# Kernel optimization log

Hardware: AMD Instinct MI355X
Metric: run time of the kernel (lower is better)

The kernel has to match this reference:

```python
import jax, jax.numpy as jnp
import numpy as np

# ---- static config (from init_kwargs) ----
SAMPLE_RATE = 2048.0
MAX_SHIFT = int(0.025 * SAMPLE_RATE)          # 51 samples
NUM_BINS = 16
FFTLENGTH = 1.0                               # chisq_kernel_length (s)
DF = 1.0 / FFTLENGTH
NUM_FREQS = int(FFTLENGTH * SAMPLE_RATE // 2 + 1)   # 1025 == rfft bins of 2048 samples
HIGHPASS = 32.0
CHISQ_PENALTY = 1.0
_freqs = np.arange(NUM_FREQS) / FFTLENGTH
MASK = _freqs >= HIGHPASS                     # static numpy bool mask

BATCH, CHANNELS, DIM = 256, 2, 2048


def setup_inputs() -> dict:
    key = jax.random.key(0)
    k1, k2 = jax.random.split(key)
    x_hat = jax.random.normal(k1, (BATCH, CHANNELS, DIM), dtype=jnp.float32)
    x = jax.random.normal(k2, (BATCH, CHANNELS, DIM), dtype=jnp.float32)
    return {"x_hat": x_hat, "x": x}


def _center(x):
    xmin = x.min(-1, keepdims=True)
    xmax = x.max(-1, keepdims=True)
    return 2 * (x - xmin) / (xmax - xmin) - 1


def _shifted_pearson(x, y, max_shift):
    # x, y: [B, C, T]; returns corr: [W, B, C] with W = 2*max_shift + 1
    b, c, t = x.shape
    num_windows = 2 * max_shift + 1
    xp = jnp.pad(x, ((0, 0), (0, 0), (max_shift, max_shift)))
    # window w, position i -> xp[..., i + w]  (same layout as torch unfold)
    idx = jnp.arange(num_windows)[:, None] + jnp.arange(t)[None, :]   # [W, T]
    xw = xp[:, :, idx]                                                # [B, C, W, T]
    xw = jnp.transpose(xw, (2, 0, 1, 3))                              # [W, B, C, T]
    xw = xw - xw.mean(-1, keepdims=True)
    yc = y - y.mean(-1, keepdims=True)
    corr = (xw * yc).sum(-1)
    norm = (xw ** 2).sum(-1) * (yc ** 2).sum(-1)
    return corr / jnp.sqrt(norm)


def _snr_integral(a, b):
    # |4 * a * conj(b) * df| cumulatively summed over frequency
    integrand = a * jnp.conj(b)
    return jnp.abs(4 * integrand * DF).cumsum(-1)


def _chisq(htilde, stilde):
    htilde = htilde[:, :, MASK]
    stilde = stilde[:, :, MASK]
    # partition frequencies by the template's own optimal-SNR integral
    si = _snr_integral(htilde, htilde)                    # [B, C, F]
    total = si[:, :, -1:]
    bins = (jnp.arange(NUM_BINS + 1, dtype=si.dtype) / NUM_BINS) * total  # [B, C, NB+1]
    search = jax.vmap(jax.vmap(lambda a, v: jnp.searchsorted(a, v, side="right")))
    edges = search(si, bins)
    edges = jnp.clip(edges, 0, si.shape[-1] - 1)
    qtilde = htilde / jnp.sqrt(total).astype(htilde.dtype)
    # SNR per bin of the normalized template against the strain
    si2 = _snr_integral(qtilde, stilde)                   # [B, C, F]
    total2 = si2[:, :, -1:]
    right = jnp.take_along_axis(si2, edges[:, :, 1:], axis=-1)
    left = jnp.take_along_axis(si2, edges[:, :, :-1], axis=-1)
    snr_per_bin = right - left                            # [B, C, NB]
    summand = (snr_per_bin - total2 / NUM_BINS) ** 2
    chisq = NUM_BINS * summand.sum(-1) / (NUM_BINS - 1)
    return total2[:, :, 0], chisq


def reference(x_hat, x):
    x_hat = _center(x_hat)
    corr = _shifted_pearson(x_hat, x, MAX_SHIFT)          # [W, B, C]
    corr = corr.max(0)                                    # [B, C]
    loss = (1 - corr) / (1 + corr)
    htilde = jnp.fft.rfft(x_hat, axis=-1) / SAMPLE_RATE   # [B, C, 1025] complex
    stilde = jnp.fft.rfft(x, axis=-1) / SAMPLE_RATE
    _, chisq = _chisq(htilde, stilde)
    chisq = chisq * CHISQ_PENALTY
    loss = loss * (1 + chisq ** 3) ** (1.0 / 6.0)
    return loss
```

## Files before the change

kernel.cpp:

```cpp
#include <hip/hip_runtime.h>
#include <math.h>

#define ROWS 512
#define DIM 2048
#define MS 51
#define NWIN 103
#define KMIN 32
#define NMASK 993

__global__ __launch_bounds__(512) void fused_mfl_kernel(
    const float* __restrict__ xhat, const float* __restrict__ x,
    float* __restrict__ out)
{
    const int r = blockIdx.x;
    const int t = threadIdx.x;
    const int lane = t & 63;
    const int wave = t >> 6;

    __shared__ float smem[13056];
    float2* A2  = (float2*)smem;
    float2* B2  = (float2*)(smem + 4096);
    float2* TW  = (float2*)(smem + 8192);
    float2* Qlo = (float2*)smem;
    float2* Qhi = (float2*)smem + 1024;
    float* siA  = smem + 4096;
    float* siBr = smem + 5120;
    float* red6 = smem + 9216;
    float* ah   = smem + 12288;
    float* xhd  = smem + 12339;
    float* at_  = smem + 12390;
    float* xt_  = smem + 12441;
    float* Ah   = smem + 12492;
    float* Aqh  = smem + 12544;
    float* Xh   = smem + 12596;
    float* At   = smem + 12648;
    float* Aqt  = smem + 12700;
    float* Xt   = smem + 12752;
    float* corrv= smem + 12804;
    float* accv = smem + 12907;

    __shared__ float sc[8];
    __shared__ int   edges[17];
    __shared__ float summ[16];
    __shared__ float wsA[4], wsB[4];

    const float* xhp = xhat + (size_t)r * DIM;
    const float* xrp = x    + (size_t)r * DIM;
    float av[4] = {xhp[t], xhp[t+512], xhp[t+1024], xhp[t+1536]};
    float bv[4] = {xrp[t], xrp[t+512], xrp[t+1024], xrp[t+1536]};

    float swv, cwv;
    sincosf((float)t * (-3.14159265358979323846f / 1024.0f), &swv, &cwv);
    TW[t] = make_float2(cwv, swv);

    {
        float mn4 = fminf(fminf(av[0],av[1]), fminf(av[2],av[3]));
        float mx4 = fmaxf(fmaxf(av[0],av[1]), fmaxf(av[2],av[3]));
        float sa = (av[0]+av[1])+(av[2]+av[3]);
        float qa = (av[0]*av[0]+av[1]*av[1])+(av[2]*av[2]+av[3]*av[3]);
        float sx = (bv[0]+bv[1])+(bv[2]+bv[3]);
        float qx = (bv[0]*bv[0]+bv[1]*bv[1])+(bv[2]*bv[2]+bv[3]*bv[3]);
        red6[t] = mn4; red6[512+t] = mx4; red6[1024+t] = sa;
        red6[1536+t] = qa; red6[2048+t] = sx; red6[2560+t] = qx;
    }
    if (t < MS)   { ah[t] = av[0];      xhd[t] = bv[0]; }
    if (t >= 461) { at_[t-461] = av[3]; xt_[t-461] = bv[3]; }
    {
        float t0r=av[0]+av[2], t0i=bv[0]+bv[2];
        float t1r=av[0]-av[2], t1i=bv[0]-bv[2];
        float t2r=av[1]+av[3], t2i=bv[1]+bv[3];
        float d3r=av[1]-av[3], d3i=bv[1]-bv[3];
        float t3r=d3i, t3i=-d3r;
        float w1r=cwv, w1i=swv;
        float w2r=w1r*w1r-w1i*w1i, w2i=2.f*w1r*w1i;
        float w3r=w2r*w1r-w2i*w1i, w3i=w2r*w1i+w2i*w1r;
        float y0r=t0r+t2r, y0i=t0i+t2i;
        float a1r=t1r+t3r, a1i=t1i+t3i;
        float y1r=a1r*w1r-a1i*w1i, y1i=a1r*w1i+a1i*w1r;
        float a2r=t0r-t2r, a2i=t0i-t2i;
        float y2r=a2r*w2r-a2i*w2i, y2i=a2r*w2i+a2i*w2r;
        float a3r=t1r-t3r, a3i=t1i-t3i;
        float y3r=a3r*w3r-a3i*w3i, y3i=a3r*w3i+a3i*w3r;
        B2[4*t]   = make_float2(y0r,y0i);
        B2[4*t+1] = make_float2(y1r,y1i);
        B2[4*t+2] = make_float2(y2r,y2i);
        B2[4*t+3] = make_float2(y3r,y3i);
    }
    __syncthreads();

    auto fft2048 = [&](const float2* Sp, float2* Dp, const int s) {
        const int q = t;
        const int u = q & ~(s - 1);
        float2 x0 = Sp[q], x1 = Sp[q+512], x2 = Sp[q+1024], x3 = Sp[q+1536];
        float t0r=x0.x+x2.x, t0i=x0.y+x2.y;
        float t1r=x0.x-x2.x, t1i=x0.y-x2.y;
        float t2r=x1.x+x3.x, t2i=x1.y+x3.y;
        float d3r=x1.x-x3.x, d3i=x1.y-x3.y;
        float t3r=d3i, t3i=-d3r;
        float2 w1 = TW[u];
        float w2r=w1.x*w1.x-w1.y*w1.y, w2i=2.f*w1.x*w1.y;
        float w3r=w2r*w1.x-w2i*w1.y,  w3i=w2r*w1.y+w2i*w1.x;
        float y0r=t0r+t2r, y0i=t0i+t2i;
        float a1r=t1r+t3r, a1i=t1i+t3i;
        float y1r=a1r*w1.x-a1i*w1.y, y1i=a1r*w1.y+a1i*w1.x;
        float a2r=t0r-t2r, a2i=t0i-t2i;
        float y2r=a2r*w2r-a2i*w2i, y2i=a2r*w2i+a2i*w2r;
        float a3r=t1r-t3r, a3i=t1i-t3i;
        float y3r=a3r*w3r-a3i*w3i, y3i=a3r*w3i+a3i*w3r;
        int base = q + 3*u;
        Dp[base]     = make_float2(y0r,y0i);
        Dp[base+s]   = make_float2(y1r,y1i);
        Dp[base+2*s] = make_float2(y2r,y2i);
        Dp[base+3*s] = make_float2(y3r,y3i);
    };
    auto fft1024 = [&](const float2* Sp, float2* Dp, const int s) {
        const int q = t;
        const int u = q & ~(s - 1);
        float2 x0 = Sp[q], x1 = Sp[q+256], x2 = Sp[q+512], x3 = Sp[q+768];
        float t0r=x0.x+x2.x, t0i=x0.y+x2.y;
        float t1r=x0.x-x2.x, t1i=x0.y-x2.y;
        float t2r=x1.x+x3.x, t2i=x1.y+x3.y;
        float d3r=x1.x-x3.x, d3i=x1.y-x3.y;
        float t3r=d3i, t3i=-d3r;
        float2 w1 = TW[2*u];
        float w2r=w1.x*w1.x-w1.y*w1.y, w2i=2.f*w1.x*w1.y;
        float w3r=w2r*w1.x-w2i*w1.y,  w3i=w2r*w1.y+w2i*w1.x;
        float y0r=t0r+t2r, y0i=t0i+t2i;
        float a1r=t1r+t3r, a1i=t1i+t3i;
        float y1r=a1r*w1.x-a1i*w1.y, y1i=a1r*w1.y+a1i*w1.x;
        float a2r=t0r-t2r, a2i=t0i-t2i;
        float y2r=a2r*w2r-a2i*w2i, y2i=a2r*w2i+a2i*w2r;
        float a3r=t1r-t3r, a3i=t1i-t3i;
        float y3r=a3r*w3r-a3i*w3i, y3i=a3r*w3i+a3i*w3r;
        int base = q + 3*u;
        Dp[base]     = make_float2(y0r,y0i);
        Dp[base+s]   = make_float2(y1r,y1i);
        Dp[base+2*s] = make_float2(y2r,y2i);
        Dp[base+3*s] = make_float2(y3r,y3i);
    };

    fft2048(B2, A2, 4);
    if (wave == 0) {
        float4 u, v;
        u=((const float4*)(red6     ))[2*lane]; v=((const float4*)(red6     ))[2*lane+1];
        float pmn=fminf(fminf(fminf(u.x,u.y),fminf(u.z,u.w)),fminf(fminf(v.x,v.y),fminf(v.z,v.w)));
        u=((const float4*)(red6+ 512))[2*lane]; v=((const float4*)(red6+ 512))[2*lane+1];
        float pmx=fmaxf(fmaxf(fmaxf(u.x,u.y),fmaxf(u.z,u.w)),fmaxf(fmaxf(v.x,v.y),fmaxf(v.z,v.w)));
        u=((const float4*)(red6+1024))[2*lane]; v=((const float4*)(red6+1024))[2*lane+1];
        float psa=((u.x+u.y)+(u.z+u.w))+((v.x+v.y)+(v.z+v.w));
        u=((const float4*)(red6+1536))[2*lane]; v=((const float4*)(red6+1536))[2*lane+1];
        float pqa=((u.x+u.y)+(u.z+u.w))+((v.x+v.y)+(v.z+v.w));
        u=((const float4*)(red6+2048))[2*lane]; v=((const float4*)(red6+2048))[2*lane+1];
        float psx=((u.x+u.y)+(u.z+u.w))+((v.x+v.y)+(v.z+v.w));
        u=((const float4*)(red6+2560))[2*lane]; v=((const float4*)(red6+2560))[2*lane+1];
        float pqx=((u.x+u.y)+(u.z+u.w))+((v.x+v.y)+(v.z+v.w));
#pragma unroll
        for (int d = 32; d; d >>= 1) {
            pmn=fminf(pmn,__shfl_down(pmn,d)); pmx=fmaxf(pmx,__shfl_down(pmx,d));
            psa+=__shfl_down(psa,d); pqa+=__shfl_down(pqa,d);
            psx+=__shfl_down(psx,d); pqx+=__shfl_down(pqx,d);
        }
        if (lane == 0) {
            float scl = 2.0f/(pmx - pmn);
            float Cc  = scl*pmn + 1.0f;
            float mean = psx * (1.0f/DIM);
            sc[0]=scl; sc[1]=Cc; sc[2]=mean; sc[3]=psa; sc[4]=pqa;
            sc[5]=pqx - (float)DIM*mean*mean;
        }
    } else if (wave == 2) {
        float va=0.f, vq=0.f, vx=0.f;
        if (lane >= 1 && lane <= MS) { float aa=ah[lane-1]; va=aa; vq=aa*aa; vx=xhd[lane-1]; }
#pragma unroll
        for (int d = 1; d < 64; d <<= 1) {
            float ya=__shfl_up(va,d), yq=__shfl_up(vq,d), yx=__shfl_up(vx,d);
            if (lane >= d) { va+=ya; vq+=yq; vx+=yx; }
        }
        if (lane <= MS) { Ah[lane]=va; Aqh[lane]=vq; Xh[lane]=vx; }
    } else if (wave == 3) {
        float va=0.f, vq=0.f, vx=0.f;
        if (lane >= 1 && lane <= MS) { float aa=at_[MS-lane]; va=aa; vq=aa*aa; vx=xt_[MS-lane]; }
#pragma unroll
        for (int d = 1; d < 64; d <<= 1) {
            float ya=__shfl_up(va,d), yq=__shfl_up(vq,d), yx=__shfl_up(vx,d);
            if (lane >= d) { va+=ya; vq+=yq; vx+=yx; }
        }
        if (lane <= MS) { At[lane]=va; Aqt[lane]=vq; Xt[lane]=vx; }
    }
    __syncthreads();
    fft2048(A2, B2, 16);  __syncthreads();
    fft2048(B2, A2, 64);  __syncthreads();
    fft2048(A2, B2, 256); __syncthreads();

    const float scl = sc[0], Cc = sc[1], mean = sc[2];
    const float Sa = sc[3], Qa = sc[4], Szz = sc[5];
    const float MSC = 0.5f * (1.0f / 2048.0f);

    float se0=0,se1=0,se2=0,se3=0, sg0=0,sg1=0,sg2=0,sg3=0;
    float incE=0, incG=0, totE=0, totG=0;

    if (t < 256) {
        const int q = t;
        float2 wA = TW[q], wB = TW[q + 256];
        auto mkQ = [&](int k, float2 w, int ni) -> float2 {
            float2 Pa, Pb;
            if (k == 0) {
                float2 U = B2[0], V = B2[1024];
                float drx = U.x - V.x, dry = U.y - V.y;
                Pa = make_float2(0.f, 0.f);
                Pb = make_float2(4.f * drx * dry, 0.f);
            } else {
                float2 U = B2[k], V = B2[k + 1024];
                float2 R = B2[1024 - k], T = B2[2048 - k];
                float zfr = U.x + V.x, zfi = U.y + V.y;
                float zgr = R.x - T.x, zgi = R.y - T.y;
                float hre = zfr + zgr, him = zfi - zgi;
                float sre = zfi + zgi, sim = zgr - zfr;
                Pa = make_float2(hre*sre + him*sim, -(him*sre - hre*sim));
                float zfr2 = R.x + T.x, zfi2 = R.y + T.y;
                float zgr2 = U.x - V.x, zgi2 = U.y - V.y;
                float hre2 = zfr2 + zgr2, him2 = zfi2 - zgi2;
                float sre2 = zfi2 + zgi2, sim2 = zgr2 - zfr2;
                Pb = make_float2(hre2*sre2 + him2*sim2, him2*sre2 - hre2*sim2);
            }
            float D1r = Pa.x + Pb.x, D1i = Pa.y + Pb.y;
            float D2r = Pa.x - Pb.x, D2i = Pa.y - Pb.y;
            float Er = D2r*w.x - D2i*w.y;
            float Ei = D2r*w.y + D2i*w.x;
            if (ni) return make_float2(D1r - Er, D1i - Ei);
            return make_float2(D1r + Ei, D1i - Er);
        };
        float2 x0 = mkQ(q,     wA, 0);
        float2 x1 = mkQ(q+256, wB, 0);
        float2 x2 = mkQ(q+512, wA, 1);
        float2 x3 = mkQ(q+768, wB, 1);
        float t0r=x0.x+x2.x, t0i=x0.y+x2.y;
        float t1r=x0.x-x2.x, t1i=x0.y-x2.y;
        float t2r=x1.x+x3.x, t2i=x1.y+x3.y;
        float d3r=x1.x-x3.x, d3i=x1.y-x3.y;
        float t3r=d3i, t3i=-d3r;
        float2 w1 = TW[2*q];
        float w2r=w1.x*w1.x-w1.y*w1.y, w2i=2.f*w1.x*w1.y;
        float w3r=w2r*w1.x-w2i*w1.y,  w3i=w2r*w1.y+w2i*w1.x;
        float y0r=t0r+t2r, y0i=t0i+t2i;
        float a1r=t1r+t3r, a1i=t1i+t3i;
        float y1r=a1r*w1.x-a1i*w1.y, y1i=a1r*w1.y+a1i*w1.x;
        float a2r=t0r-t2r, a2i=t0i-t2i;
        float y2r=a2r*w2r-a2i*w2i, y2i=a2r*w2i+a2i*w2r;
        float a3r=t1r-t3r, a3i=t1i-t3i;
        float y3r=a3r*w3r-a3i*w3i, y3i=a3r*w3i+a3i*w3r;
        Qlo[4*q]   = make_float2(y0r,y0i);
        Qlo[4*q+1] = make_float2(y1r,y1i);
        Qlo[4*q+2] = make_float2(y2r,y2i);
        Qlo[4*q+3] = make_float2(y3r,y3i);
    } else {
        int tt = t - 256;
        float ee[4], gg[4];
#pragma unroll
        for (int j = 0; j < 4; ++j) {
            int m = 4*tt + j;
            ee[j] = 0.f; gg[j] = 0.f;
            if (m < NMASK) {
                int f = m + KMIN;
                float zfr, zfi;
                if (f < 1024) { float2 U=B2[f], V=B2[f+1024]; zfr=U.x+V.x; zfi=U.y+V.y; }
                else          { float2 U=B2[0], V=B2[1024];   zfr=U.x-V.x; zfi=U.y-V.y; }
                int gi = 2048 - f;
                float2 p2 = B2[gi-1024], q3 = B2[gi];
                float zgr = p2.x - q3.x, zgi = p2.y - q3.y;
                float hre = zfr + zgr, him = zfi - zgi;
                float sre = zfi + zgi, sim = zgr - zfr;
                float hm = scl * sqrtf(hre*hre + him*him) * MSC;
                float sm = sqrtf(sre*sre + sim*sim) * MSC;
                ee[j] = 4.f*hm*hm; gg[j] = 4.f*hm*sm;
            }
        }
        se0=ee[0]; se1=se0+ee[1]; se2=se1+ee[2]; se3=se2+ee[3];
        sg0=gg[0]; sg1=sg0+gg[1]; sg2=sg1+gg[2]; sg3=sg2+gg[3];
        totE=se3; totG=sg3; incE=totE; incG=totG;
#pragma unroll
        for (int d = 1; d < 64; d <<= 1) {
            float yE=__shfl_up(incE,d), yG=__shfl_up(incG,d);
            if (lane >= d) { incE+=yE; incG+=yG; }
        }
        if (lane == 63) { wsA[wave-4]=incE; wsB[wave-4]=incG; }
    }
    __syncthreads();

    if (t < 256) { fft1024(Qlo, Qhi, 4); }
    else {
        int tt = t - 256, w4 = wave - 4;
        float offE=0.f, offG=0.f;
        for (int w = 0; w < w4; ++w) { offE+=wsA[w]; offG+=wsB[w]; }
        float preE = offE + incE - totE;
        float preG = offG + incG - totG;
        ((float4*)siA)[tt]  = make_float4(preE+se0, preE+se1, preE+se2, preE+se3);
        ((float4*)siBr)[tt] = make_float4(preG+sg0, preG+sg1, preG+sg2, preG+sg3);
    }
    __syncthreads();

    if (t < 256) { fft1024(Qhi, Qlo, 16); }
    else if (t < 256 + 17) {
        int tl = t - 256;
        float total = siA[NMASK-1];
        float bin = ((float)tl * (1.0f/16.0f)) * total;
        int lo = 0, hi = NMASK;
        while (lo < hi) { int mid=(lo+hi)>>1; if (siA[mid] <= bin) lo=mid+1; else hi=mid; }
        edges[tl] = (lo < NMASK-1) ? lo : (NMASK-1);
    }
    __syncthreads();

    if (t < 256) { fft1024(Qlo, Qhi, 64); }
    else {
        int idx = t - 256;
        if (idx < 16) {
            float total = siA[NMASK-1];
            float qf = 1.0f / sqrtf(total);
            float total2 = siBr[NMASK-1] * qf;
            float snr = (siBr[edges[idx+1]] - siBr[edges[idx]]) * qf;
            float d = snr - total2 * (1.0f/16.0f);
            summ[idx] = d * d;
        }
        int c = idx >> 1, k2 = idx & 1;
        if (c < NWIN) {
            int off = c - MS;
            float acc = 0.f;
            if (off > 0) {
                for (int j = k2; j < off; j += 2) acc += ah[j] * (xt_[MS-off+j] - mean);
            } else if (off < 0) {
                int o = -off;
                for (int j = k2; j < o; j += 2) acc += at_[MS-o+j] * (xhd[j] - mean);
            }
            acc += __shfl_down(acc, 1);
            if (k2 == 0) accv[c] = acc;
        }
    }
    __syncthreads();

    if (t < NWIN) {
        int c = t;
        int off = c - MS;
        int sidx = (off >= 0) ? off : (2048 + off);
        int n = sidx >> 1;
        int q = n & 255;
        float2 x0 = Qhi[q], x1 = Qhi[q+256], x2 = Qhi[q+512], x3 = Qhi[q+768];
        float2 Fv;
        if (n < 256) {
            Fv = make_float2((x0.x+x2.x)+(x1.x+x3.x), (x0.y+x2.y)+(x1.y+x3.y));
        } else {
            float t1r_ = x0.x - x2.x, t1i_ = x0.y - x2.y;
            float d3r_ = x1.x - x3.x, d3i_ = x1.y - x3.y;
            Fv = make_float2(t1r_ - d3i_, t1i_ + d3r_);
        }
        float val = (sidx & 1) ? -Fv.y : Fv.x;
        float circ = val * (1.0f/8192.0f);
        float acc = accv[c];
        float Sin_a, Sin_q, Zex, nin;
        if (off >= 0) {
            Sin_a = Sa - Ah[off]; Sin_q = Qa - Aqh[off];
            Zex = Xt[off] - (float)off * mean; nin = 2048.0f - (float)off;
        } else {
            int o = -off;
            Sin_a = Sa - At[o]; Sin_q = Qa - Aqt[o];
            Zex = Xh[o] - (float)o * mean; nin = 2048.0f - (float)o;
        }
        float num = scl * (circ - acc) + Cc * Zex;
        float Sw  = scl * Sin_a - Cc * nin;
        float Sw2 = scl*scl*Sin_q - 2.f*scl*Cc*Sin_a + Cc*Cc*nin;
        float varw = Sw2 - Sw * Sw * (1.0f/2048.0f);
        corrv[c] = num / sqrtf(varw * Szz);
    }
    __syncthreads();

    if (wave == 0) {
        float m = corrv[lane];
        if (lane + 64 < NWIN) m = fmaxf(m, corrv[lane + 64]);
#pragma unroll
        for (int d = 32; d; d >>= 1) m = fmaxf(m, __shfl_down(m, d));
        if (lane == 0) {
            float loss0 = (1.0f - m) / (1.0f + m);
            float ss = 0.f;
            for (int i = 0; i < 16; ++i) ss += summ[i];
            float chisq = 16.0f * ss / 15.0f;
            float c3 = chisq * chisq * chisq;
            out[r] = loss0 * powf(1.0f + c3, 1.0f/6.0f);
        }
    }
}

extern "C" void kernel_launch(void* const* d_in, const int* in_sizes, int n_in,
                              void* d_out, int out_size, void* d_ws, size_t ws_size,
                              hipStream_t stream) {
    const float* xhat = (const float*)d_in[0];
    const float* x    = (const float*)d_in[1];
    float* out = (float*)d_out;
    (void)in_sizes; (void)n_in; (void)out_size; (void)d_ws; (void)ws_size;

    fused_mfl_kernel<<<ROWS, 512, 0, stream>>>(xhat, x, out);
}
```

Before: 67.23 us.

## Switch 2048-point FFT to radix-8 stages and simplify spectrum unpacking

Replaces the three remaining radix-4 passes of the 2048-point complex FFT with two radix-8 passes run by 256 threads. This removes one LDS round trip and one block barrier. The scalar reductions and prefix scans move to waves 4-6 so they overlap with the FFT. Spectrum unpacking now reads the final output directly instead of recombining half-size results, and sincosf/powf become fast intrinsics. In exchange, half the block sits idle during the FFT passes, and the fast intrinsics lose a little precision.

Result: faster. 65.75 us (-2.2%).

```diff
diff --git a/kernel.cpp b/kernel.cpp
--- a/kernel.cpp
+++ b/kernel.cpp
@@ -50,7 +50,7 @@
     float bv[4] = {xrp[t], xrp[t+512], xrp[t+1024], xrp[t+1536]};
 
     float swv, cwv;
-    sincosf((float)t * (-3.14159265358979323846f / 1024.0f), &swv, &cwv);
+    __sincosf((float)t * (-3.14159265358979323846f / 1024.0f), &swv, &cwv);
     TW[t] = make_float2(cwv, swv);
 
     {
@@ -81,37 +81,77 @@
         float y2r=a2r*w2r-a2i*w2i, y2i=a2r*w2i+a2i*w2r;
         float a3r=t1r-t3r, a3i=t1i-t3i;
         float y3r=a3r*w3r-a3i*w3i, y3i=a3r*w3i+a3i*w3r;
-        B2[4*t]   = make_float2(y0r,y0i);
-        B2[4*t+1] = make_float2(y1r,y1i);
-        B2[4*t+2] = make_float2(y2r,y2i);
-        B2[4*t+3] = make_float2(y3r,y3i);
-    }
-    __syncthreads();
-
-    auto fft2048 = [&](const float2* Sp, float2* Dp, const int s) {
+        A2[4*t]   = make_float2(y0r,y0i);
+        A2[4*t+1] = make_float2(y1r,y1i);
+        A2[4*t+2] = make_float2(y2r,y2i);
+        A2[4*t+3] = make_float2(y3r,y3i);
+    }
+    __syncthreads();
+
+    auto fft2048_r8 = [&](const float2* Sp, float2* Dp, const int s, const bool tw) {
         const int q = t;
         const int u = q & ~(s - 1);
-        float2 x0 = Sp[q], x1 = Sp[q+512], x2 = Sp[q+1024], x3 = Sp[q+1536];
-        float t0r=x0.x+x2.x, t0i=x0.y+x2.y;
-        float t1r=x0.x-x2.x, t1i=x0.y-x2.y;
-        float t2r=x1.x+x3.x, t2i=x1.y+x3.y;
-        float d3r=x1.x-x3.x, d3i=x1.y-x3.y;
-        float t3r=d3i, t3i=-d3r;
-        float2 w1 = TW[u];
-        float w2r=w1.x*w1.x-w1.y*w1.y, w2i=2.f*w1.x*w1.y;
-        float w3r=w2r*w1.x-w2i*w1.y,  w3i=w2r*w1.y+w2i*w1.x;
-        float y0r=t0r+t2r, y0i=t0i+t2i;
-        float a1r=t1r+t3r, a1i=t1i+t3i;
-        float y1r=a1r*w1.x-a1i*w1.y, y1i=a1r*w1.y+a1i*w1.x;
-        float a2r=t0r-t2r, a2i=t0i-t2i;
-        float y2r=a2r*w2r-a2i*w2i, y2i=a2r*w2i+a2i*w2r;
-        float a3r=t1r-t3r, a3i=t1i-t3i;
-        float y3r=a3r*w3r-a3i*w3i, y3i=a3r*w3i+a3i*w3r;
-        int base = q + 3*u;
-        Dp[base]     = make_float2(y0r,y0i);
-        Dp[base+s]   = make_float2(y1r,y1i);
-        Dp[base+2*s] = make_float2(y2r,y2i);
-        Dp[base+3*s] = make_float2(y3r,y3i);
+        float2 x0=Sp[q],      x1=Sp[q+256],  x2=Sp[q+512],  x3=Sp[q+768];
+        float2 x4=Sp[q+1024], x5=Sp[q+1280], x6=Sp[q+1536], x7=Sp[q+1792];
+        float e0r=x0.x+x4.x, e0i=x0.y+x4.y;
+        float e1r=x0.x-x4.x, e1i=x0.y-x4.y;
+        float e2r=x2.x+x6.x, e2i=x2.y+x6.y;
+        float e3r=x2.x-x6.x, e3i=x2.y-x6.y;
+        float A0r=e0r+e2r, A0i=e0i+e2i;
+        float A1r=e1r+e3i, A1i=e1i-e3r;
+        float A2r_=e0r-e2r, A2i_=e0i-e2i;
+        float A3r=e1r-e3i, A3i=e1i+e3r;
+        float o0r=x1.x+x5.x, o0i=x1.y+x5.y;
+        float o1r=x1.x-x5.x, o1i=x1.y-x5.y;
+        float o2r=x3.x+x7.x, o2i=x3.y+x7.y;
+        float o3r=x3.x-x7.x, o3i=x3.y-x7.y;
+        float B0r=o0r+o2r, B0i=o0i+o2i;
+        float B1r=o1r+o3i, B1i=o1i-o3r;
+        float B2r_=o0r-o2r, B2i_=o0i-o2i;
+        float B3r=o1r-o3i, B3i=o1i+o3r;
+        const float RT = 0.70710678118654752f;
+        float C1r = RT*(B1r + B1i), C1i = RT*(B1i - B1r);
+        float C2r = B2i_,           C2i = -B2r_;
+        float C3r = RT*(B3i - B3r), C3i = -RT*(B3r + B3i);
+        float y0r=A0r+B0r,  y0i=A0i+B0i;
+        float y1r=A1r+C1r,  y1i=A1i+C1i;
+        float y2r=A2r_+C2r, y2i=A2i_+C2i;
+        float y3r=A3r+C3r,  y3i=A3i+C3i;
+        float y4r=A0r-B0r,  y4i=A0i-B0i;
+        float y5r=A1r-C1r,  y5i=A1i-C1i;
+        float y6r=A2r_-C2r, y6i=A2i_-C2i;
+        float y7r=A3r-C3r,  y7i=A3i-C3i;
+        int base = q + 7*u;
+        Dp[base] = make_float2(y0r, y0i);
+        if (tw) {
+            float2 w1 = TW[u];
+            auto cm = [](float ar, float ai, float br, float bi, float* rr, float* ri) {
+                *rr = ar*br - ai*bi; *ri = ar*bi + ai*br;
+            };
+            float w2r,w2i,w3r,w3i,w4r,w4i,w5r,w5i,w6r,w6i,w7r,w7i;
+            cm(w1.x,w1.y,w1.x,w1.y,&w2r,&w2i);
+            cm(w2r,w2i,w1.x,w1.y,&w3r,&w3i);
+            cm(w2r,w2i,w2r,w2i,&w4r,&w4i);
+            cm(w2r,w2i,w3r,w3i,&w5r,&w5i);
+            cm(w3r,w3i,w3r,w3i,&w6r,&w6i);
+            cm(w3r,w3i,w4r,w4i,&w7r,&w7i);
+            float rr, ri;
+            cm(y1r,y1i,w1.x,w1.y,&rr,&ri); Dp[base+s]   = make_float2(rr,ri);
+            cm(y2r,y2i,w2r,w2i,&rr,&ri);   Dp[base+2*s] = make_float2(rr,ri);
+            cm(y3r,y3i,w3r,w3i,&rr,&ri);   Dp[base+3*s] = make_float2(rr,ri);
+            cm(y4r,y4i,w4r,w4i,&rr,&ri);   Dp[base+4*s] = make_float2(rr,ri);
+            cm(y5r,y5i,w5r,w5i,&rr,&ri);   Dp[base+5*s] = make_float2(rr,ri);
+            cm(y6r,y6i,w6r,w6i,&rr,&ri);   Dp[base+6*s] = make_float2(rr,ri);
+            cm(y7r,y7i,w7r,w7i,&rr,&ri);   Dp[base+7*s] = make_float2(rr,ri);
+        } else {
+            Dp[base+s]   = make_float2(y1r,y1i);
+            Dp[base+2*s] = make_float2(y2r,y2i);
+            Dp[base+3*s] = make_float2(y3r,y3i);
+            Dp[base+4*s] = make_float2(y4r,y4i);
+            Dp[base+5*s] = make_float2(y5r,y5i);
+            Dp[base+6*s] = make_float2(y6r,y6i);
+            Dp[base+7*s] = make_float2(y7r,y7i);
+        }
     };
     auto fft1024 = [&](const float2* Sp, float2* Dp, const int s) {
         const int q = t;
@@ -139,8 +179,9 @@
         Dp[base+3*s] = make_float2(y3r,y3i);
     };
 
-    fft2048(B2, A2, 4);
-    if (wave == 0) {
+    if (t < 256) {
+        fft2048_r8(A2, B2, 4, true);
+    } else if (wave == 4) {
         float4 u, v;
         u=((const float4*)(red6     ))[2*lane]; v=((const float4*)(red6     ))[2*lane+1];
         float pmn=fminf(fminf(fminf(u.x,u.y),fminf(u.z,u.w)),fminf(fminf(v.x,v.y),fminf(v.z,v.w)));
@@ -167,7 +208,7 @@
             sc[0]=scl; sc[1]=Cc; sc[2]=mean; sc[3]=psa; sc[4]=pqa;
             sc[5]=pqx - (float)DIM*mean*mean;
         }
-    } else if (wave == 2) {
+    } else if (wave == 5) {
         float va=0.f, vq=0.f, vx=0.f;
         if (lane >= 1 && lane <= MS) { float aa=ah[lane-1]; va=aa; vq=aa*aa; vx=xhd[lane-1]; }
 #pragma unroll
@@ -176,7 +217,7 @@
             if (lane >= d) { va+=ya; vq+=yq; vx+=yx; }
         }
         if (lane <= MS) { Ah[lane]=va; Aqh[lane]=vq; Xh[lane]=vx; }
-    } else if (wave == 3) {
+    } else if (wave == 6) {
         float va=0.f, vq=0.f, vx=0.f;
         if (lane >= 1 && lane <= MS) { float aa=at_[MS-lane]; va=aa; vq=aa*aa; vx=xt_[MS-lane]; }
 #pragma unroll
@@ -187,9 +228,10 @@
         if (lane <= MS) { At[lane]=va; Aqt[lane]=vq; Xt[lane]=vx; }
     }
     __syncthreads();
-    fft2048(A2, B2, 16);  __syncthreads();
-    fft2048(B2, A2, 64);  __syncthreads();
-    fft2048(A2, B2, 256); __syncthreads();
+    if (t < 256) { fft2048_r8(B2, A2, 32, true); }
+    __syncthreads();
+    if (t < 256) { fft2048_r8(A2, B2, 256, false); }
+    __syncthreads();
 
     const float scl = sc[0], Cc = sc[1], mean = sc[2];
     const float Sa = sc[3], Qa = sc[4], Szz = sc[5];
@@ -204,22 +246,17 @@
         auto mkQ = [&](int k, float2 w, int ni) -> float2 {
             float2 Pa, Pb;
             if (k == 0) {
-                float2 U = B2[0], V = B2[1024];
-                float drx = U.x - V.x, dry = U.y - V.y;
+                float2 Xm = B2[1024];
                 Pa = make_float2(0.f, 0.f);
-                Pb = make_float2(4.f * drx * dry, 0.f);
+                Pb = make_float2(4.f * Xm.x * Xm.y, 0.f);
             } else {
-                float2 U = B2[k], V = B2[k + 1024];
-                float2 R = B2[1024 - k], T = B2[2048 - k];
-                float zfr = U.x + V.x, zfi = U.y + V.y;
-                float zgr = R.x - T.x, zgi = R.y - T.y;
-                float hre = zfr + zgr, him = zfi - zgi;
-                float sre = zfi + zgi, sim = zgr - zfr;
+                float2 Xk = B2[k], Xn = B2[2048-k];
+                float hre = Xk.x + Xn.x, him = Xk.y - Xn.y;
+                float sre = Xk.y + Xn.y, sim = Xn.x - Xk.x;
                 Pa = make_float2(hre*sre + him*sim, -(him*sre - hre*sim));
-                float zfr2 = R.x + T.x, zfi2 = R.y + T.y;
-                float zgr2 = U.x - V.x, zgi2 = U.y - V.y;
-                float hre2 = zfr2 + zgr2, him2 = zfi2 - zgi2;
-                float sre2 = zfi2 + zgi2, sim2 = zgr2 - zfr2;
+                float2 Xm = B2[1024-k], Xp = B2[1024+k];
+                float hre2 = Xm.x + Xp.x, him2 = Xm.y - Xp.y;
+                float sre2 = Xm.y + Xp.y, sim2 = Xp.x - Xm.x;
                 Pb = make_float2(hre2*sre2 + him2*sim2, him2*sre2 - hre2*sim2);
             }
             float D1r = Pa.x + Pb.x, D1i = Pa.y + Pb.y;
@@ -261,14 +298,9 @@
             ee[j] = 0.f; gg[j] = 0.f;
             if (m < NMASK) {
                 int f = m + KMIN;
-                float zfr, zfi;
-                if (f < 1024) { float2 U=B2[f], V=B2[f+1024]; zfr=U.x+V.x; zfi=U.y+V.y; }
-                else          { float2 U=B2[0], V=B2[1024];   zfr=U.x-V.x; zfi=U.y-V.y; }
-                int gi = 2048 - f;
-                float2 p2 = B2[gi-1024], q3 = B2[gi];
-                float zgr = p2.x - q3.x, zgi = p2.y - q3.y;
-                float hre = zfr + zgr, him = zfi - zgi;
-                float sre = zfi + zgi, sim = zgr - zfr;
+                float2 Xf = B2[f], Xg = B2[2048-f];
+                float hre = Xf.x + Xg.x, him = Xf.y - Xg.y;
+                float sre = Xf.y + Xg.y, sim = Xg.x - Xf.x;
                 float hm = scl * sqrtf(hre*hre + him*him) * MSC;
                 float sm = sqrtf(sre*sre + sim*sim) * MSC;
                 ee[j] = 4.f*hm*hm; gg[j] = 4.f*hm*sm;
@@ -382,7 +414,7 @@
             for (int i = 0; i < 16; ++i) ss += summ[i];
             float chisq = 16.0f * ss / 15.0f;
             float c3 = chisq * chisq * chisq;
-            out[r] = loss0 * powf(1.0f + c3, 1.0f/6.0f);
+            out[r] = loss0 * __powf(1.0f + c3, 1.0f/6.0f);
         }
     }
 }
```
